# Kernel optimization log

Hardware: AMD Instinct MI355X
Metric: run time of the kernel (lower is better)

## Reference

```python
import jax, jax.numpy as jnp
import numpy as np

LN_EPS = 1e-5
SUM_CLAMP = 1e-12


def setup_inputs() -> dict:
    key = jax.random.key(0)
    ks = jax.random.split(key, 10)
    L, D, H, P, E = 200000, 512, 512, 16384, 200000
    lesion_x = jax.random.normal(ks[0], (L, D), dtype=jnp.float32)
    edge_index = jnp.stack([
        jax.random.randint(ks[1], (E,), 0, P),   # patient idx
        jax.random.randint(ks[2], (E,), 0, L),   # lesion idx
    ], axis=0).astype(jnp.int64)
    s1 = 1.0 / np.sqrt(D)
    s2 = 1.0 / np.sqrt(H)
    W1 = jax.random.uniform(ks[3], (H, D), jnp.float32, -s1, s1)
    b1 = jax.random.uniform(ks[4], (H,), jnp.float32, -s1, s1)
    W2 = jax.random.uniform(ks[5], (1, H), jnp.float32, -s2, s2)
    b2 = jax.random.uniform(ks[6], (1,), jnp.float32, -s2, s2)
    Wp = jax.random.uniform(ks[7], (768, D), jnp.float32, -s1, s1)
    bp = jax.random.uniform(ks[8], (768,), jnp.float32, -s1, s1)
    gamma = jnp.ones((768,), jnp.float32)
    beta = jnp.zeros((768,), jnp.float32)
    return dict(lesion_x=lesion_x, patient_to_lesion_edge_index=edge_index,
                num_patients_in_batch=P, W1=W1, b1=b1, W2=W2, b2=b2,
                Wp=Wp, bp=bp, gamma=gamma, beta=beta)


def reference(lesion_x, patient_to_lesion_edge_index, num_patients_in_batch,
              W1, b1, W2, b2, Wp, bp, gamma, beta):
    P = int(num_patients_in_batch)
    pat = patient_to_lesion_edge_index[0]
    les = patient_to_lesion_edge_index[1]
    feats = lesion_x[les]                                  # [E, D] gather
    h = jnp.tanh(feats @ W1.T + b1)                        # [E, H]
    scores = (h @ W2.T + b2)[:, 0]                         # [E]
    smax = jax.ops.segment_max(scores, pat, num_segments=P)  # [P]
    ex = jnp.exp(scores - smax[pat])                       # [E]
    esum = jax.ops.segment_sum(ex, pat, num_segments=P)
    esum = jnp.maximum(esum, SUM_CLAMP)
    alpha = ex / esum[pat]                                 # [E]
    agg = jax.ops.segment_sum(feats * alpha[:, None], pat, num_segments=P)  # [P, D]
    proj = agg @ Wp.T + bp                                 # [P, 768]
    mu = jnp.mean(proj, axis=-1, keepdims=True)
    var = jnp.mean(jnp.square(proj - mu), axis=-1, keepdims=True)
    out = (proj - mu) * jax.lax.rsqrt(var + LN_EPS) * gamma + beta
    return out
```

## Files before the change

kernel.cpp:

```cpp
#include <hip/hip_runtime.h>
#include <hip/hip_bf16.h>

#define D_DIM 512
#define H_DIM 512
#define O_DIM 768

using bf16x8 = __attribute__((ext_vector_type(8))) short;
using f32x4  = __attribute__((ext_vector_type(4))) float;

static __device__ __forceinline__ unsigned short f2bf(float f){
  unsigned u = __float_as_uint(f);
  u += 0x7fffu + ((u >> 16) & 1u);
  return (unsigned short)(u >> 16);
}

static __device__ __forceinline__ unsigned cvtpk(float lo, float hi){
  unsigned r;
  asm("v_cvt_pk_bf16_f32 %0, %1, %2" : "=v"(r) : "v"(lo), "v"(hi));
  return r;
}

static __device__ __forceinline__ float bflo(unsigned u){
  return __uint_as_float(u << 16);
}
static __device__ __forceinline__ float bfhi(unsigned u){
  return __uint_as_float(u & 0xffff0000u);
}

static __device__ __forceinline__ float fast_tanh(float x){
  float e = __expf(2.f * x);
  return 1.f - 2.f / (e + 1.f);
}

static __device__ __forceinline__ unsigned f2ord(float f){
  unsigned u = __float_as_uint(f);
  return (u & 0x80000000u) ? ~u : (u | 0x80000000u);
}
static __device__ __forceinline__ float ord2f(unsigned u){
  u = (u & 0x80000000u) ? (u & 0x7fffffffu) : ~u;
  return __uint_as_float(u);
}

static __device__ __forceinline__ void gload16(const void* g, void* l){
  __builtin_amdgcn_global_load_lds(
      (const __attribute__((address_space(1))) void*)g,
      (__attribute__((address_space(3))) void*)l, 16, 0, 0);
}

__global__ void cvt_bf16(const float* __restrict__ in,
                         unsigned short* __restrict__ out, int n8)
{
  int stride = gridDim.x * blockDim.x;
  for (int i = blockIdx.x*blockDim.x + threadIdx.x; i < n8; i += stride){
    const float4* p = (const float4*)in + (size_t)i*2;
    float4 a = p[0], b = p[1];
    uint4 pk = { cvtpk(a.x,a.y) | 0u, 0u, 0u, 0u };
    pk.x = cvtpk(a.x, a.y);
    pk.y = cvtpk(a.z, a.w);
    pk.z = cvtpk(b.x, b.y);
    pk.w = cvtpk(b.z, b.w);
    ((uint4*)out)[i] = pk;
  }
}

__launch_bounds__(256, 3)
__global__ void gemm1_rs(const float* __restrict__ A,
                         const short* __restrict__ Bm,
                         const float* __restrict__ bias,
                         const float* __restrict__ w2,
                         float* __restrict__ out,
                         short* __restrict__ Ab,
                         int M, int nwg)
{
  __shared__ short lds_a[128*64];
  __shared__ short lds_b[128*64];

  const int q  = nwg >> 3, rr = nwg & 7;
  const int xcd = blockIdx.x & 7, bidx = blockIdx.x >> 3;
  const int swz = (xcd < rr ? xcd*(q+1) : rr*(q+1) + (xcd-rr)*q) + bidx;
  const int colBase = (swz & 3) * 128;
  const int rowBase = (swz >> 2) * 128;
  const bool writeAb = (colBase == 0);

  const int tid  = threadIdx.x;
  const int lane = tid & 63;
  const int w    = tid >> 6;
  const int wr   = w >> 1, wc = w & 1;
  const int lr   = lane & 15;
  const int lk   = lane >> 4;

  const int srow = tid >> 4;
  const int sgf  = tid & 15;
  const int rlocB = lane >> 3;
  const int jB    = lane & 7;

  f32x4 acc[4][4];
  #pragma unroll
  for (int i = 0; i < 4; ++i)
    #pragma unroll
    for (int j = 0; j < 4; ++j)
      acc[i][j] = (f32x4){0.f, 0.f, 0.f, 0.f};

  for (int kt = 0; kt < 512/64; ++kt){
    const int kOff = kt * 64;
    #pragma unroll
    for (int c = 0; c < 4; ++c){
      int rt = w*32 + c*8 + rlocB;
      int js = jB ^ (rt & 7);
      gload16(Bm + (size_t)(colBase + rt)*512 + kOff + js*8,
              &lds_b[(w*32 + c*8)*64]);
    }
    float4 va[8];
    #pragma unroll
    for (int c = 0; c < 8; ++c){
      int gA = rowBase + c*16 + srow; if (gA > M-1) gA = M-1;
      va[c] = *(const float4*)(A + (size_t)gA*512 + kOff + sgf*4);
    }
    #pragma unroll
    for (int c = 0; c < 8; ++c){
      int rt = c*16 + srow;
      uint2 pk = { cvtpk(va[c].x, va[c].y), cvtpk(va[c].z, va[c].w) };
      int sidx = (rt*64 + sgf*4) ^ ((rt & 7) << 3);
      *(uint2*)&lds_a[sidx] = pk;
      if (writeAb){
        int gA = rowBase + rt;
        if (gA < M) *(uint2*)(Ab + (size_t)gA*512 + kOff + sgf*4) = pk;
      }
    }
    __syncthreads();
    #pragma unroll
    for (int kk = 0; kk < 2; ++kk){
      bf16x8 af[4], bfr[4];
      #pragma unroll
      for (int mf = 0; mf < 4; ++mf){
        int r   = wr*64 + mf*16 + lr;
        int idx = (r*64 + kk*32 + lk*8) ^ ((r & 7) << 3);
        af[mf] = *(bf16x8*)&lds_a[idx];
      }
      #pragma unroll
      for (int nf = 0; nf < 4; ++nf){
        int r   = wc*64 + nf*16 + lr;
        int idx = (r*64 + kk*32 + lk*8) ^ ((r & 7) << 3);
        bfr[nf] = *(bf16x8*)&lds_b[idx];
      }
      #pragma unroll
      for (int mf = 0; mf < 4; ++mf)
        #pragma unroll
        for (int nf = 0; nf < 4; ++nf)
          acc[mf][nf] = __builtin_amdgcn_mfma_f32_16x16x32_bf16(
              af[mf], bfr[nf], acc[mf][nf], 0, 0, 0);
    }
    __syncthreads();
  }

  #pragma unroll
  for (int mf = 0; mf < 4; ++mf){
    float part[4] = {0.f,0.f,0.f,0.f};
    #pragma unroll
    for (int nf = 0; nf < 4; ++nf){
      int gc = colBase + wc*64 + nf*16 + lr;
      float b = bias[gc], wv = w2[gc];
      #pragma unroll
      for (int r = 0; r < 4; ++r)
        part[r] += fast_tanh(acc[mf][nf][r] + b) * wv;
    }
    #pragma unroll
    for (int r = 0; r < 4; ++r){
      part[r] += __shfl_xor(part[r], 1);
      part[r] += __shfl_xor(part[r], 2);
      part[r] += __shfl_xor(part[r], 4);
      part[r] += __shfl_xor(part[r], 8);
    }
    if (lr == 0){
      int gr = rowBase + wr*64 + mf*16 + lk*4;
      #pragma unroll
      for (int r = 0; r < 4; ++r)
        if (gr + r < M) atomicAdd(&out[gr + r], part[r]);
    }
  }
}

__launch_bounds__(256, 2)
__global__ void gemm2_bf16(const short* __restrict__ A,
                           const short* __restrict__ Bm,
                           const float* __restrict__ bias,
                           float* __restrict__ out,
                           int M, int outStride)
{
  __shared__ short lds_a[128*64];
  __shared__ short lds_b[128*64];

  const int tid  = threadIdx.x;
  const int lane = tid & 63;
  const int w    = tid >> 6;
  const int wr   = w >> 1, wc = w & 1;
  const int lr   = lane & 15;
  const int lk   = lane >> 4;

  const int colBase = blockIdx.x * 128;
  const int rowBase = blockIdx.y * 128;

  f32x4 acc[4][4];
  #pragma unroll
  for (int i = 0; i < 4; ++i)
    #pragma unroll
    for (int j = 0; j < 4; ++j)
      acc[i][j] = (f32x4){0.f, 0.f, 0.f, 0.f};

  const int subrow = lane >> 3;
  const int gpre   = lane & 7;

  for (int kt = 0; kt < 512/64; ++kt){
    const int kOff = kt * 64;
    #pragma unroll
    for (int c = 0; c < 4; ++c){
      int r    = w*32 + c*8 + subrow;
      int gran = gpre ^ (r & 7);
      int gA   = rowBase + r; if (gA > M-1) gA = M-1;
      gload16(A  + (size_t)gA*512 + kOff + gran*8, &lds_a[(w*32 + c*8)*64]);
      int gB   = colBase + r;
      gload16(Bm + (size_t)gB*512 + kOff + gran*8, &lds_b[(w*32 + c*8)*64]);
    }
    __syncthreads();
    #pragma unroll
    for (int kk = 0; kk < 2; ++kk){
      bf16x8 af[4], bfr[4];
      #pragma unroll
      for (int mf = 0; mf < 4; ++mf){
        int r   = wr*64 + mf*16 + lr;
        int idx = (r*64 + kk*32 + lk*8) ^ ((r & 7) << 3);
        af[mf] = *(bf16x8*)&lds_a[idx];
      }
      #pragma unroll
      for (int nf = 0; nf < 4; ++nf){
        int r   = wc*64 + nf*16 + lr;
        int idx = (r*64 + kk*32 + lk*8) ^ ((r & 7) << 3);
        bfr[nf] = *(bf16x8*)&lds_b[idx];
      }
      #pragma unroll
      for (int mf = 0; mf < 4; ++mf)
        #pragma unroll
        for (int nf = 0; nf < 4; ++nf)
          acc[mf][nf] = __builtin_amdgcn_mfma_f32_16x16x32_bf16(
              af[mf], bfr[nf], acc[mf][nf], 0, 0, 0);
    }
    __syncthreads();
  }

  #pragma unroll
  for (int mf = 0; mf < 4; ++mf){
    int gr = rowBase + wr*64 + mf*16 + lk*4;
    #pragma unroll
    for (int nf = 0; nf < 4; ++nf){
      int gc = colBase + wc*64 + nf*16 + lr;
      float b = bias[gc];
      #pragma unroll
      for (int r = 0; r < 4; ++r)
        if (gr + r < M) out[(size_t)(gr + r)*outStride + gc] = acc[mf][nf][r] + b;
    }
  }
}

__global__ void edge_pass1(const int* __restrict__ edge, int E,
                           const float* __restrict__ scores,
                           unsigned* __restrict__ smax_o,
                           int* __restrict__ hist)
{
  int e = blockIdx.x*256 + threadIdx.x;
  if (e >= E) return;
  int p = edge[e], l = edge[E + e];
  atomicMax(&smax_o[p], f2ord(scores[l]));
  atomicAdd(&hist[p], 1);
}

__global__ void scan_kernel(const int* __restrict__ hist,
                            int* __restrict__ offsets, int P)
{
  __shared__ int s[1024];
  int t = threadIdx.x;
  int local[16]; int sum = 0;
  #pragma unroll
  for (int i = 0; i < 16; ++i){
    int idx = t*16 + i;
    local[i] = (idx < P) ? hist[idx] : 0;
    sum += local[i];
  }
  s[t] = sum;
  __syncthreads();
  for (int off = 1; off < 1024; off <<= 1){
    int v = (t >= off) ? s[t - off] : 0;
    __syncthreads();
    s[t] += v;
    __syncthreads();
  }
  int run = s[t] - sum;
  #pragma unroll
  for (int i = 0; i < 16; ++i){
    int idx = t*16 + i;
    if (idx < P) offsets[idx] = run;
    run += local[i];
  }
}

__global__ void edge_pass2(const int* __restrict__ edge, int E,
                           const float* __restrict__ scores,
                           const unsigned* __restrict__ smax_o,
                           float* __restrict__ ex,
                           float* __restrict__ esum,
                           const int* __restrict__ offsets,
                           int* __restrict__ cursor,
                           int* __restrict__ sorted)
{
  int e = blockIdx.x*256 + threadIdx.x;
  if (e >= E) return;
  int p = edge[e], l = edge[E + e];
  float v = __expf(scores[l] - ord2f(smax_o[p]));
  ex[e] = v;
  atomicAdd(&esum[p], v);
  int pos = atomicAdd(&cursor[p], 1);
  sorted[offsets[p] + pos] = e;
}

__global__ void agg_kernel(const int* __restrict__ edge, int E,
                           const short* __restrict__ Ab,
                           const float* __restrict__ ex,
                           const float* __restrict__ esum,
                           const int* __restrict__ offsets,
                           const int* __restrict__ hist,
                           const int* __restrict__ sorted,
                           unsigned* __restrict__ aggb)
{
  int p    = blockIdx.x*4 + (threadIdx.x >> 6);
  int lane = threadIdx.x & 63;
  int n = hist[p];
  if (n == 0) return;
  int start = offsets[p];
  float inv = 1.f / fmaxf(esum[p], 1e-12f);
  float a[8] = {0.f,0.f,0.f,0.f,0.f,0.f,0.f,0.f};
  for (int i = 0; i < n; ++i){
    int e = sorted[start + i];
    int l = edge[E + e];
    float alpha = ex[e] * inv;
    uint4 u = *(const uint4*)(Ab + (size_t)l*512 + lane*8);
    a[0] += alpha * bflo(u.x);  a[1] += alpha * bfhi(u.x);
    a[2] += alpha * bflo(u.y);  a[3] += alpha * bfhi(u.y);
    a[4] += alpha * bflo(u.z);  a[5] += alpha * bfhi(u.z);
    a[6] += alpha * bflo(u.w);  a[7] += alpha * bfhi(u.w);
  }
  uint4 o = { cvtpk(a[0],a[1]), cvtpk(a[2],a[3]),
              cvtpk(a[4],a[5]), cvtpk(a[6],a[7]) };
  *(uint4*)&aggb[(size_t)p*256 + lane*4] = o;
}

__global__ void ln_kernel(float* __restrict__ out,
                          const float* __restrict__ gamma,
                          const float* __restrict__ beta)
{
  __shared__ float red1[4];
  __shared__ float red2[4];
  int p = blockIdx.x;
  float* row = out + (size_t)p*768;
  int t = threadIdx.x;
  float v0 = row[t], v1 = row[t+256], v2 = row[t+512];
  float s = v0 + v1 + v2;
  #pragma unroll
  for (int off = 32; off; off >>= 1) s += __shfl_down(s, off);
  int lane = t & 63, wv = t >> 6;
  if (lane == 0) red1[wv] = s;
  __syncthreads();
  float mean = (red1[0]+red1[1]+red1[2]+red1[3]) * (1.f/768.f);
  float d0 = v0-mean, d1 = v1-mean, d2 = v2-mean;
  float qq = d0*d0 + d1*d1 + d2*d2;
  #pragma unroll
  for (int off = 32; off; off >>= 1) qq += __shfl_down(qq, off);
  if (lane == 0) red2[wv] = qq;
  __syncthreads();
  float var = (red2[0]+red2[1]+red2[2]+red2[3]) * (1.f/768.f);
  float inv = rsqrtf(var + 1e-5f);
  row[t]     = d0*inv*gamma[t]     + beta[t];
  row[t+256] = d1*inv*gamma[t+256] + beta[t+256];
  row[t+512] = d2*inv*gamma[t+512] + beta[t+512];
}

extern "C" void kernel_launch(void* const* d_in, const int* in_sizes, int n_in,
                              void* d_out, int out_size, void* d_ws, size_t ws_size,
                              hipStream_t stream)
{
  const float* lesion_x = (const float*)d_in[0];
  const int*   edge     = (const int*)d_in[1];
  const float* W1    = (const float*)d_in[3];
  const float* b1    = (const float*)d_in[4];
  const float* W2    = (const float*)d_in[5];
  const float* Wp    = (const float*)d_in[7];
  const float* bp    = (const float*)d_in[8];
  const float* gamma = (const float*)d_in[9];
  const float* beta  = (const float*)d_in[10];

  const int L = in_sizes[0] / D_DIM;
  const int E = in_sizes[1] / 2;
  const int P = out_size / O_DIM;

  auto al = [](size_t x){ return (x + 255) & ~(size_t)255; };
  char* ws = (char*)d_ws;
  size_t oScores = 0;
  size_t oSmax   = oScores + al((size_t)L*4);
  size_t oEsum   = oSmax   + al((size_t)P*4);
  size_t oHist   = oEsum   + al((size_t)P*4);
  size_t oCursor = oHist   + al((size_t)P*4);
  size_t smallEnd= oCursor + al((size_t)P*4);
  size_t oAggB   = smallEnd;
  size_t aggEnd  = oAggB   + al((size_t)P*D_DIM*2);
  size_t oOff    = aggEnd;
  size_t oEx     = oOff    + al((size_t)P*4);
  size_t oSorted = oEx     + al((size_t)E*4);
  size_t oW1b    = oSorted + al((size_t)E*4);
  size_t oWpb    = oW1b    + al((size_t)H_DIM*D_DIM*2);
  size_t oAb     = oWpb    + al((size_t)O_DIM*D_DIM*2);
  size_t need    = oAb     + al((size_t)L*D_DIM*2);
  (void)need;

  float*    scores = (float*)(ws + oScores);
  unsigned* smax_o = (unsigned*)(ws + oSmax);
  float*    esum   = (float*)(ws + oEsum);
  int*      hist   = (int*)(ws + oHist);
  int*      cursor = (int*)(ws + oCursor);
  unsigned* aggb   = (unsigned*)(ws + oAggB);
  int*      offs   = (int*)(ws + oOff);
  float*    ex     = (float*)(ws + oEx);
  int*      sorted = (int*)(ws + oSorted);
  short*    W1b    = (short*)(ws + oW1b);
  short*    Wpb    = (short*)(ws + oWpb);
  short*    Ab     = (short*)(ws + oAb);

  hipMemsetAsync(d_ws, 0, smallEnd, stream);
  hipMemsetAsync(ws + oAggB, 0, (size_t)P*D_DIM*2, stream);

  dim3 b256(256);
  int eb = (E + 255) / 256;

  cvt_bf16<<<128, b256, 0, stream>>>(W1, (unsigned short*)W1b, H_DIM*D_DIM/8);
  cvt_bf16<<<192, b256, 0, stream>>>(Wp, (unsigned short*)Wpb, O_DIM*D_DIM/8);

  int nRow = (L + 127) / 128;
  int nwg  = 4 * nRow;
  gemm1_rs<<<nwg, b256, 0, stream>>>(lesion_x, W1b, b1, W2, scores, Ab, L, nwg);

  edge_pass1<<<eb, b256, 0, stream>>>(edge, E, scores, smax_o, hist);
  scan_kernel<<<1, 1024, 0, stream>>>(hist, offs, P);
  edge_pass2<<<eb, b256, 0, stream>>>(edge, E, scores, smax_o, ex, esum,
                                      offs, cursor, sorted);
  agg_kernel<<<P/4, b256, 0, stream>>>(edge, E, Ab, ex, esum, offs,
                                       hist, sorted, aggb);
  gemm2_bf16<<<dim3(O_DIM/128, P/128), b256, 0, stream>>>(
      (const short*)aggb, Wpb, bp, (float*)d_out, P, O_DIM);
  ln_kernel<<<P, b256, 0, stream>>>((float*)d_out, gamma, beta);
}
```

Baseline: 413.7 us.

## Double-buffer LDS in gemm1 and prefetch next gathered row in aggregation

The first GEMM now uses two LDS buffers per operand. The next K-tile's A loads and async B loads are issued before the current tile's MFMAs, and the converted A data is written into the other buffer afterwards, so one barrier per iteration replaces two. MFMA sections get raised wave priority via s_setprio. Occupancy hint drops from 3 to 2 blocks because LDS doubles. The aggregation kernel software-prefetches the next edge's gathered row and weight to hide gather latency.

```diff
diff --git a/kernel.cpp b/kernel.cpp
--- a/kernel.cpp
+++ b/kernel.cpp
@@ -7,12 +7,6 @@
 
 using bf16x8 = __attribute__((ext_vector_type(8))) short;
 using f32x4  = __attribute__((ext_vector_type(4))) float;
-
-static __device__ __forceinline__ unsigned short f2bf(float f){
-  unsigned u = __float_as_uint(f);
-  u += 0x7fffu + ((u >> 16) & 1u);
-  return (unsigned short)(u >> 16);
-}
 
 static __device__ __forceinline__ unsigned cvtpk(float lo, float hi){
   unsigned r;
@@ -54,7 +48,7 @@
   for (int i = blockIdx.x*blockDim.x + threadIdx.x; i < n8; i += stride){
     const float4* p = (const float4*)in + (size_t)i*2;
     float4 a = p[0], b = p[1];
-    uint4 pk = { cvtpk(a.x,a.y) | 0u, 0u, 0u, 0u };
+    uint4 pk;
     pk.x = cvtpk(a.x, a.y);
     pk.y = cvtpk(a.z, a.w);
     pk.z = cvtpk(b.x, b.y);
@@ -63,8 +57,8 @@
   }
 }
 
-__launch_bounds__(256, 3)
-__global__ void gemm1_rs(const float* __restrict__ A,
+__launch_bounds__(256, 2)
+__global__ void gemm1_db(const float* __restrict__ A,
                          const short* __restrict__ Bm,
                          const float* __restrict__ bias,
                          const float* __restrict__ w2,
@@ -72,8 +66,8 @@
                          short* __restrict__ Ab,
                          int M, int nwg)
 {
-  __shared__ short lds_a[128*64];
-  __shared__ short lds_b[128*64];
+  __shared__ short lds_a[2][128*64];
+  __shared__ short lds_b[2][128*64];
 
   const int q  = nwg >> 3, rr = nwg & 7;
   const int xcd = blockIdx.x & 7, bidx = blockIdx.x >> 3;
@@ -101,33 +95,50 @@
     for (int j = 0; j < 4; ++j)
       acc[i][j] = (f32x4){0.f, 0.f, 0.f, 0.f};
 
-  for (int kt = 0; kt < 512/64; ++kt){
-    const int kOff = kt * 64;
-    #pragma unroll
-    for (int c = 0; c < 4; ++c){
-      int rt = w*32 + c*8 + rlocB;
-      int js = jB ^ (rt & 7);
-      gload16(Bm + (size_t)(colBase + rt)*512 + kOff + js*8,
-              &lds_b[(w*32 + c*8)*64]);
-    }
-    float4 va[8];
-    #pragma unroll
-    for (int c = 0; c < 8; ++c){
-      int gA = rowBase + c*16 + srow; if (gA > M-1) gA = M-1;
-      va[c] = *(const float4*)(A + (size_t)gA*512 + kOff + sgf*4);
-    }
-    #pragma unroll
-    for (int c = 0; c < 8; ++c){
-      int rt = c*16 + srow;
-      uint2 pk = { cvtpk(va[c].x, va[c].y), cvtpk(va[c].z, va[c].w) };
-      int sidx = (rt*64 + sgf*4) ^ ((rt & 7) << 3);
-      *(uint2*)&lds_a[sidx] = pk;
-      if (writeAb){
-        int gA = rowBase + rt;
-        if (gA < M) *(uint2*)(Ab + (size_t)gA*512 + kOff + sgf*4) = pk;
-      }
-    }
-    __syncthreads();
+  float4 va[8];
+
+  #pragma unroll
+  for (int c = 0; c < 8; ++c){
+    int gA = rowBase + c*16 + srow; if (gA > M-1) gA = M-1;
+    va[c] = *(const float4*)(A + (size_t)gA*512 + sgf*4);
+  }
+  #pragma unroll
+  for (int c = 0; c < 4; ++c){
+    int rt = w*32 + c*8 + rlocB;
+    int js = jB ^ (rt & 7);
+    gload16(Bm + (size_t)(colBase + rt)*512 + js*8, &lds_b[0][(w*32 + c*8)*64]);
+  }
+  #pragma unroll
+  for (int c = 0; c < 8; ++c){
+    int rt = c*16 + srow;
+    uint2 pk = { cvtpk(va[c].x, va[c].y), cvtpk(va[c].z, va[c].w) };
+    int sidx = (rt*64 + sgf*4) ^ ((rt & 7) << 3);
+    *(uint2*)&lds_a[0][sidx] = pk;
+    if (writeAb){
+      int gA = rowBase + rt;
+      if (gA < M) *(uint2*)(Ab + (size_t)gA*512 + sgf*4) = pk;
+    }
+  }
+  __syncthreads();
+
+  int cur = 0;
+  for (int kt = 0; kt < 8; ++kt){
+    const int nxt = cur ^ 1;
+    const int kNext = (kt + 1) * 64;
+    if (kt < 7){
+      #pragma unroll
+      for (int c = 0; c < 8; ++c){
+        int gA = rowBase + c*16 + srow; if (gA > M-1) gA = M-1;
+        va[c] = *(const float4*)(A + (size_t)gA*512 + kNext + sgf*4);
+      }
+      #pragma unroll
+      for (int c = 0; c < 4; ++c){
+        int rt = w*32 + c*8 + rlocB;
+        int js = jB ^ (rt & 7);
+        gload16(Bm + (size_t)(colBase + rt)*512 + kNext + js*8,
+                &lds_b[nxt][(w*32 + c*8)*64]);
+      }
+    }
     #pragma unroll
     for (int kk = 0; kk < 2; ++kk){
       bf16x8 af[4], bfr[4];
@@ -135,22 +146,38 @@
       for (int mf = 0; mf < 4; ++mf){
         int r   = wr*64 + mf*16 + lr;
         int idx = (r*64 + kk*32 + lk*8) ^ ((r & 7) << 3);
-        af[mf] = *(bf16x8*)&lds_a[idx];
+        af[mf] = *(bf16x8*)&lds_a[cur][idx];
       }
       #pragma unroll
       for (int nf = 0; nf < 4; ++nf){
         int r   = wc*64 + nf*16 + lr;
         int idx = (r*64 + kk*32 + lk*8) ^ ((r & 7) << 3);
-        bfr[nf] = *(bf16x8*)&lds_b[idx];
-      }
+        bfr[nf] = *(bf16x8*)&lds_b[cur][idx];
+      }
+      __builtin_amdgcn_s_setprio(1);
       #pragma unroll
       for (int mf = 0; mf < 4; ++mf)
         #pragma unroll
         for (int nf = 0; nf < 4; ++nf)
           acc[mf][nf] = __builtin_amdgcn_mfma_f32_16x16x32_bf16(
               af[mf], bfr[nf], acc[mf][nf], 0, 0, 0);
+      __builtin_amdgcn_s_setprio(0);
+    }
+    if (kt < 7){
+      #pragma unroll
+      for (int c = 0; c < 8; ++c){
+        int rt = c*16 + srow;
+        uint2 pk = { cvtpk(va[c].x, va[c].y), cvtpk(va[c].z, va[c].w) };
+        int sidx = (rt*64 + sgf*4) ^ ((rt & 7) << 3);
+        *(uint2*)&lds_a[nxt][sidx] = pk;
+        if (writeAb){
+          int gA = rowBase + rt;
+          if (gA < M) *(uint2*)(Ab + (size_t)gA*512 + kNext + sgf*4) = pk;
+        }
+      }
     }
     __syncthreads();
+    cur = nxt;
   }
 
   #pragma unroll
@@ -337,15 +364,20 @@
   int start = offsets[p];
   float inv = 1.f / fmaxf(esum[p], 1e-12f);
   float a[8] = {0.f,0.f,0.f,0.f,0.f,0.f,0.f,0.f};
+  int e0 = sorted[start];
+  uint4 u = *(const uint4*)(Ab + (size_t)edge[E + e0]*512 + lane*8);
+  float alpha = ex[e0] * inv;
   for (int i = 0; i < n; ++i){
-    int e = sorted[start + i];
-    int l = edge[E + e];
-    float alpha = ex[e] * inv;
-    uint4 u = *(const uint4*)(Ab + (size_t)l*512 + lane*8);
-    a[0] += alpha * bflo(u.x);  a[1] += alpha * bfhi(u.x);
-    a[2] += alpha * bflo(u.y);  a[3] += alpha * bfhi(u.y);
-    a[4] += alpha * bflo(u.z);  a[5] += alpha * bfhi(u.z);
-    a[6] += alpha * bflo(u.w);  a[7] += alpha * bfhi(u.w);
+    uint4 uc = u; float ac = alpha;
+    if (i + 1 < n){
+      int e2 = sorted[start + i + 1];
+      u = *(const uint4*)(Ab + (size_t)edge[E + e2]*512 + lane*8);
+      alpha = ex[e2] * inv;
+    }
+    a[0] += ac * bflo(uc.x);  a[1] += ac * bfhi(uc.x);
+    a[2] += ac * bflo(uc.y);  a[3] += ac * bfhi(uc.y);
+    a[4] += ac * bflo(uc.z);  a[5] += ac * bfhi(uc.z);
+    a[6] += ac * bflo(uc.w);  a[7] += ac * bfhi(uc.w);
   }
   uint4 o = { cvtpk(a[0],a[1]), cvtpk(a[2],a[3]),
               cvtpk(a[4],a[5]), cvtpk(a[6],a[7]) };
@@ -443,7 +475,7 @@
 
   int nRow = (L + 127) / 128;
   int nwg  = 4 * nRow;
-  gemm1_rs<<<nwg, b256, 0, stream>>>(lesion_x, W1b, b1, W2, scores, Ab, L, nwg);
+  gemm1_db<<<nwg, b256, 0, stream>>>(lesion_x, W1b, b1, W2, scores, Ab, L, nwg);
 
   edge_pass1<<<eb, b256, 0, stream>>>(edge, E, scores, smax_o, hist);
   scan_kernel<<<1, 1024, 0, stream>>>(hist, offs, P);
```

New measurement: 469.9 us. +13.6%, slower.

## Widen gemm1 tile to 256 columns, boost MFMA priority, prefetch in aggregation

Applied to the files above, without the earlier changes.

The first GEMM now computes 128x256 output tiles instead of 128x128, so each workgroup reads and converts the fp32 lesion rows to bf16 half as many times across the column tiles. The cost is a bigger accumulator, double the B-tile LDS, and an occupancy hint lowered from 3 to 2. MFMA sections are wrapped in s_setprio to favour issuing matrix work. The aggregation loop now software-prefetches the next edge's gathered row and alpha, to hide the latency of the dependent index-then-row load.

```diff
diff --git a/kernel.cpp b/kernel.cpp
--- a/kernel.cpp
+++ b/kernel.cpp
@@ -7,12 +7,6 @@
 
 using bf16x8 = __attribute__((ext_vector_type(8))) short;
 using f32x4  = __attribute__((ext_vector_type(4))) float;
-
-static __device__ __forceinline__ unsigned short f2bf(float f){
-  unsigned u = __float_as_uint(f);
-  u += 0x7fffu + ((u >> 16) & 1u);
-  return (unsigned short)(u >> 16);
-}
 
 static __device__ __forceinline__ unsigned cvtpk(float lo, float hi){
   unsigned r;
@@ -54,7 +48,7 @@
   for (int i = blockIdx.x*blockDim.x + threadIdx.x; i < n8; i += stride){
     const float4* p = (const float4*)in + (size_t)i*2;
     float4 a = p[0], b = p[1];
-    uint4 pk = { cvtpk(a.x,a.y) | 0u, 0u, 0u, 0u };
+    uint4 pk;
     pk.x = cvtpk(a.x, a.y);
     pk.y = cvtpk(a.z, a.w);
     pk.z = cvtpk(b.x, b.y);
@@ -63,23 +57,23 @@
   }
 }
 
-__launch_bounds__(256, 3)
-__global__ void gemm1_rs(const float* __restrict__ A,
-                         const short* __restrict__ Bm,
-                         const float* __restrict__ bias,
-                         const float* __restrict__ w2,
-                         float* __restrict__ out,
-                         short* __restrict__ Ab,
-                         int M, int nwg)
+__launch_bounds__(256, 2)
+__global__ void gemm1_wide(const float* __restrict__ A,
+                           const short* __restrict__ Bm,
+                           const float* __restrict__ bias,
+                           const float* __restrict__ w2,
+                           float* __restrict__ out,
+                           short* __restrict__ Ab,
+                           int M, int nwg)
 {
   __shared__ short lds_a[128*64];
-  __shared__ short lds_b[128*64];
+  __shared__ short lds_b[256*64];
 
   const int q  = nwg >> 3, rr = nwg & 7;
   const int xcd = blockIdx.x & 7, bidx = blockIdx.x >> 3;
   const int swz = (xcd < rr ? xcd*(q+1) : rr*(q+1) + (xcd-rr)*q) + bidx;
-  const int colBase = (swz & 3) * 128;
-  const int rowBase = (swz >> 2) * 128;
+  const int colBase = (swz & 1) * 256;
+  const int rowBase = (swz >> 1) * 128;
   const bool writeAb = (colBase == 0);
 
   const int tid  = threadIdx.x;
@@ -94,27 +88,27 @@
   const int rlocB = lane >> 3;
   const int jB    = lane & 7;
 
-  f32x4 acc[4][4];
+  f32x4 acc[4][8];
   #pragma unroll
   for (int i = 0; i < 4; ++i)
     #pragma unroll
-    for (int j = 0; j < 4; ++j)
+    for (int j = 0; j < 8; ++j)
       acc[i][j] = (f32x4){0.f, 0.f, 0.f, 0.f};
 
   for (int kt = 0; kt < 512/64; ++kt){
     const int kOff = kt * 64;
-    #pragma unroll
-    for (int c = 0; c < 4; ++c){
-      int rt = w*32 + c*8 + rlocB;
-      int js = jB ^ (rt & 7);
-      gload16(Bm + (size_t)(colBase + rt)*512 + kOff + js*8,
-              &lds_b[(w*32 + c*8)*64]);
-    }
     float4 va[8];
     #pragma unroll
     for (int c = 0; c < 8; ++c){
       int gA = rowBase + c*16 + srow; if (gA > M-1) gA = M-1;
       va[c] = *(const float4*)(A + (size_t)gA*512 + kOff + sgf*4);
+    }
+    #pragma unroll
+    for (int c = 0; c < 8; ++c){
+      int rt = w*64 + c*8 + rlocB;
+      int js = jB ^ (rt & 7);
+      gload16(Bm + (size_t)(colBase + rt)*512 + kOff + js*8,
+              &lds_b[(w*64 + c*8)*64]);
     }
     #pragma unroll
     for (int c = 0; c < 8; ++c){
@@ -130,7 +124,7 @@
     __syncthreads();
     #pragma unroll
     for (int kk = 0; kk < 2; ++kk){
-      bf16x8 af[4], bfr[4];
+      bf16x8 af[4], bfr[8];
       #pragma unroll
       for (int mf = 0; mf < 4; ++mf){
         int r   = wr*64 + mf*16 + lr;
@@ -138,17 +132,19 @@
         af[mf] = *(bf16x8*)&lds_a[idx];
       }
       #pragma unroll
-      for (int nf = 0; nf < 4; ++nf){
-        int r   = wc*64 + nf*16 + lr;
+      for (int nf = 0; nf < 8; ++nf){
+        int r   = wc*128 + nf*16 + lr;
         int idx = (r*64 + kk*32 + lk*8) ^ ((r & 7) << 3);
         bfr[nf] = *(bf16x8*)&lds_b[idx];
       }
+      __builtin_amdgcn_s_setprio(1);
       #pragma unroll
       for (int mf = 0; mf < 4; ++mf)
         #pragma unroll
-        for (int nf = 0; nf < 4; ++nf)
+        for (int nf = 0; nf < 8; ++nf)
           acc[mf][nf] = __builtin_amdgcn_mfma_f32_16x16x32_bf16(
               af[mf], bfr[nf], acc[mf][nf], 0, 0, 0);
+      __builtin_amdgcn_s_setprio(0);
     }
     __syncthreads();
   }
@@ -157,8 +153,8 @@
   for (int mf = 0; mf < 4; ++mf){
     float part[4] = {0.f,0.f,0.f,0.f};
     #pragma unroll
-    for (int nf = 0; nf < 4; ++nf){
-      int gc = colBase + wc*64 + nf*16 + lr;
+    for (int nf = 0; nf < 8; ++nf){
+      int gc = colBase + wc*128 + nf*16 + lr;
       float b = bias[gc], wv = w2[gc];
       #pragma unroll
       for (int r = 0; r < 4; ++r)
@@ -337,15 +333,20 @@
   int start = offsets[p];
   float inv = 1.f / fmaxf(esum[p], 1e-12f);
   float a[8] = {0.f,0.f,0.f,0.f,0.f,0.f,0.f,0.f};
+  int e0 = sorted[start];
+  uint4 u = *(const uint4*)(Ab + (size_t)edge[E + e0]*512 + lane*8);
+  float alpha = ex[e0] * inv;
   for (int i = 0; i < n; ++i){
-    int e = sorted[start + i];
-    int l = edge[E + e];
-    float alpha = ex[e] * inv;
-    uint4 u = *(const uint4*)(Ab + (size_t)l*512 + lane*8);
-    a[0] += alpha * bflo(u.x);  a[1] += alpha * bfhi(u.x);
-    a[2] += alpha * bflo(u.y);  a[3] += alpha * bfhi(u.y);
-    a[4] += alpha * bflo(u.z);  a[5] += alpha * bfhi(u.z);
-    a[6] += alpha * bflo(u.w);  a[7] += alpha * bfhi(u.w);
+    uint4 uc = u; float ac = alpha;
+    if (i + 1 < n){
+      int e2 = sorted[start + i + 1];
+      u = *(const uint4*)(Ab + (size_t)edge[E + e2]*512 + lane*8);
+      alpha = ex[e2] * inv;
+    }
+    a[0] += ac * bflo(uc.x);  a[1] += ac * bfhi(uc.x);
+    a[2] += ac * bflo(uc.y);  a[3] += ac * bfhi(uc.y);
+    a[4] += ac * bflo(uc.z);  a[5] += ac * bfhi(uc.z);
+    a[6] += ac * bflo(uc.w);  a[7] += ac * bfhi(uc.w);
   }
   uint4 o = { cvtpk(a[0],a[1]), cvtpk(a[2],a[3]),
               cvtpk(a[4],a[5]), cvtpk(a[6],a[7]) };
@@ -442,8 +443,8 @@
   cvt_bf16<<<192, b256, 0, stream>>>(Wp, (unsigned short*)Wpb, O_DIM*D_DIM/8);
 
   int nRow = (L + 127) / 128;
-  int nwg  = 4 * nRow;
-  gemm1_rs<<<nwg, b256, 0, stream>>>(lesion_x, W1b, b1, W2, scores, Ab, L, nwg);
+  int nwg  = 2 * nRow;
+  gemm1_wide<<<nwg, b256, 0, stream>>>(lesion_x, W1b, b1, W2, scores, Ab, L, nwg);
 
   edge_pass1<<<eb, b256, 0, stream>>>(edge, E, scores, smax_o, hist);
   scan_kernel<<<1, 1024, 0, stream>>>(hist, offs, P);
```

Result: slower. 439.2 us (+6.2%).
